# Kernel tuning notes

Measured on AMD Instinct MI355X. Metric: run time of the kernel, lower is better.

Reference implementation:

```python
import jax, jax.numpy as jnp
import numpy as np

N = 100000  # nodes
EPS_BN = 1e-5
EPS_NORM = 1e-12


def sage_conv(x, edge_index, wl, bl, wr):
    # PyG SAGEConv (aggr='mean', normalize=True, project=False):
    # out = lin_l(mean_{j in N(i)} x_j) + lin_r(x_i); then L2-normalize rows.
    src, dst = edge_index[0], edge_index[1]
    msgs = x[src]                                            # [E, C] gather
    agg = jax.ops.segment_sum(msgs, dst, num_segments=N)     # [N, C]
    cnt = jax.ops.segment_sum(jnp.ones((edge_index.shape[1],), x.dtype), dst,
                              num_segments=N)                # [N]
    agg = agg / jnp.maximum(cnt, 1.0)[:, None]               # mean (0 for isolated)
    out = agg @ wl.T + bl + x @ wr.T                         # lin_l has bias, lin_r doesn't
    nrm = jnp.sqrt(jnp.sum(out * out, axis=-1, keepdims=True))
    return out / jnp.maximum(nrm, EPS_NORM)


def batch_norm(x, gamma, beta):
    # BatchNorm1d in training mode: batch stats, biased variance
    mean = jnp.mean(x, axis=0)
    var = jnp.mean((x - mean) ** 2, axis=0)
    return gamma * (x - mean) * jax.lax.rsqrt(var + EPS_BN) + beta


def setup_inputs() -> dict:
    key = jax.random.key(0)
    ks = jax.random.split(key, 9)
    C_in, C_h, C_out = 128, 128, 47
    E = 800000
    x = jax.random.normal(ks[0], (N, C_in), dtype=jnp.float32)
    edge_index = jax.random.randint(ks[1], (2, E), 0, N, dtype=jnp.int64)
    s = 0.1
    return {
        "x": x,
        "edge_index": edge_index,
        "w1l": jax.random.normal(ks[2], (C_h, C_in), dtype=jnp.float32) * s,
        "b1l": jnp.zeros((C_h,), dtype=jnp.float32),
        "w1r": jax.random.normal(ks[3], (C_h, C_in), dtype=jnp.float32) * s,
        "bn_gamma": jnp.ones((C_h,), dtype=jnp.float32),
        "bn_beta": jnp.zeros((C_h,), dtype=jnp.float32),
        "w2l": jax.random.normal(ks[4], (C_out, C_h), dtype=jnp.float32) * s,
        "b2l": jnp.zeros((C_out,), dtype=jnp.float32),
        "w2r": jax.random.normal(ks[5], (C_out, C_h), dtype=jnp.float32) * s,
    }


def reference(x, edge_index, w1l, b1l, w1r, bn_gamma, bn_beta, w2l, b2l, w2r):
    h = sage_conv(x, edge_index, w1l, b1l, w1r)   # [N, 128]
    h = batch_norm(h, bn_gamma, bn_beta)
    h = jax.nn.relu(h)
    # dropout p=0.0 -> identity
    out = sage_conv(h, edge_index, w2l, b2l, w2r)  # [N, 47]
    return out
```

## Files before the change

### kernel.cpp

```cpp
#include <hip/hip_runtime.h>
#include <cstdint>


typedef __attribute__((ext_vector_type(8))) short s8v;
typedef __attribute__((ext_vector_type(4))) float fx4;

#define CSR_CHUNK 8192
#define CSR_SH 8
#define CSR_NBPAD 512
#define CSR_BUFCAP 3072

static __device__ __forceinline__ float bf2f(unsigned short h) {
    union { unsigned int u; float f; } c; c.u = (unsigned int)h << 16; return c.f;
}
static __device__ __forceinline__ unsigned short f2bf(float f) {
    union { float f; unsigned int u; } c; c.f = f;
    unsigned int u = c.u;
    return (unsigned short)((u + 0x7FFF + ((u >> 16) & 1)) >> 16);
}

static __device__ __forceinline__ float warp_sum64(float v) {
    #pragma unroll
    for (int off = 32; off > 0; off >>= 1) v += __shfl_xor(v, off, 64);
    return v;
}

__global__ __launch_bounds__(256) void k_prep(
        const float* __restrict__ x, const float* __restrict__ w1l,
        const float* __restrict__ w1r, const float* __restrict__ w2l,
        const float* __restrict__ w2r, const int* __restrict__ ei,
        unsigned short* __restrict__ xb, unsigned short* __restrict__ wB1,
        unsigned short* __restrict__ wB2p, float* __restrict__ stats,
        int* __restrict__ counts, int n, int nE, int prepBlocks) {
    __shared__ int hist[CSR_NBPAD];
    int t = threadIdx.x;
    if ((int)blockIdx.x >= prepBlocks) {
        int chunk = blockIdx.x - prepBlocks;
        hist[t] = 0; hist[t + 256] = 0;
        __syncthreads();
        int e0 = chunk * CSR_CHUNK;
        int e1 = min(e0 + CSR_CHUNK, nE);
        for (int e = e0 + t; e < e1; e += 256)
            atomicAdd(&hist[ei[nE + e] >> CSR_SH], 1);
        __syncthreads();
        counts[chunk * CSR_NBPAD + t] = hist[t];
        counts[chunk * CSR_NBPAD + t + 256] = hist[t + 256];
        return;
    }
    int idx = blockIdx.x * 256 + t;
    int nx = n * 16;
    if (idx < nx) {
        float4 a = ((const float4*)x)[idx * 2];
        float4 b = ((const float4*)x)[idx * 2 + 1];
        union { s8v v; unsigned short u[8]; } o;
        o.u[0] = f2bf(a.x); o.u[1] = f2bf(a.y); o.u[2] = f2bf(a.z); o.u[3] = f2bf(a.w);
        o.u[4] = f2bf(b.x); o.u[5] = f2bf(b.y); o.u[6] = f2bf(b.z); o.u[7] = f2bf(b.w);
        ((s8v*)xb)[idx] = o.v;
        return;
    }
    idx -= nx;
    if (idx < 32768) {
        int j = idx >> 8, k = idx & 255;
        float v = (k < 128) ? w1l[j * 128 + k] : w1r[j * 128 + (k - 128)];
        wB1[idx] = f2bf(v);
        return;
    }
    idx -= 32768;
    if (idx < 16384) {
        int j = idx >> 7, k = idx & 127;
        float v = 0.f;
        if (j < 47)      v = w2l[j * 128 + k];
        else if (j < 94) v = w2r[(j - 47) * 128 + k];
        wB2p[idx] = f2bf(v);
        return;
    }
    idx -= 16384;
    if (idx < 256) stats[idx] = 0.f;
}

__global__ __launch_bounds__(256) void k_bmeta(
        const int* __restrict__ counts, int* __restrict__ bucketStart,
        int* __restrict__ gcur, int nCh, int NB) {
    __shared__ int tot[CSR_NBPAD], tot2[CSR_NBPAD], sh[256], bs[CSR_NBPAD];
    int t = threadIdx.x;
    int tl = t & 127, g = t >> 7;
    int half = (nCh + 1) >> 1;
    int c0 = g * half, c1 = min(nCh, c0 + half);
    int4 s4 = {0, 0, 0, 0};
    for (int c = c0; c < c1; ++c) {
        int4 v = *(const int4*)(counts + (size_t)c * CSR_NBPAD + tl * 4);
        s4.x += v.x; s4.y += v.y; s4.z += v.z; s4.w += v.w;
    }
    *(int4*)((g ? tot2 : tot) + tl * 4) = s4;
    __syncthreads();
    tot[t] += tot2[t];
    tot[t + 256] += tot2[t + 256];
    __syncthreads();
    int pairSum = tot[2 * t] + tot[2 * t + 1];
    sh[t] = pairSum;
    __syncthreads();
    for (int off = 1; off < 256; off <<= 1) {
        int add = (t >= off) ? sh[t - off] : 0;
        __syncthreads();
        sh[t] += add;
        __syncthreads();
    }
    int excl = sh[t] - pairSum;
    bs[2 * t] = excl;
    bs[2 * t + 1] = excl + tot[2 * t];
    __syncthreads();
    for (int b = t; b <= NB; b += 256) bucketStart[b] = bs[b];
    for (int b = t; b < CSR_NBPAD; b += 256) gcur[b] = bs[b];
}

__global__ __launch_bounds__(256) void k_bfill(
        const int* __restrict__ ei, const int* __restrict__ counts,
        int* __restrict__ gcur, int* __restrict__ pairs, int nE) {
    __shared__ int cur[CSR_NBPAD];
    int t = threadIdx.x;
    #pragma unroll
    for (int i = 0; i < 2; ++i) {
        int b = t + i * 256;
        int h = counts[blockIdx.x * CSR_NBPAD + b];
        cur[b] = h ? atomicAdd(&gcur[b], h) : 0;
    }
    __syncthreads();
    int e0 = blockIdx.x * CSR_CHUNK;
    int e1 = min(e0 + CSR_CHUNK, nE);
    for (int e = e0 + t; e < e1; e += 256) {
        int s = ei[e];
        int d = ei[nE + e];
        int p = atomicAdd(&cur[d >> CSR_SH], 1);
        pairs[p] = (s << 8) | (d & 255);
    }
}

__global__ __launch_bounds__(256) void k_csr(
        const int* __restrict__ pairs, const int* __restrict__ bucketStart,
        int* __restrict__ deg, int* __restrict__ rowStart,
        int* __restrict__ srcIdx, int n) {
    __shared__ int cnt[256], scn[256], cur[256];
    __shared__ int buf[CSR_BUFCAP];
    int t = threadIdx.x;
    int bkt = blockIdx.x;
    int eBeg = bucketStart[bkt], eEnd = bucketStart[bkt + 1];
    int node0 = bkt << CSR_SH;
    cnt[t] = 0;
    __syncthreads();
    for (int e = eBeg + t; e < eEnd; e += 256)
        atomicAdd(&cnt[pairs[e] & 255], 1);
    __syncthreads();
    int myc = cnt[t];
    scn[t] = myc;
    __syncthreads();
    for (int off = 1; off < 256; off <<= 1) {
        int add = (t >= off) ? scn[t - off] : 0;
        __syncthreads();
        scn[t] += add;
        __syncthreads();
    }
    int excl = scn[t] - myc;
    cur[t] = excl;
    int node = node0 + t;
    if (node < n) { deg[node] = myc; rowStart[node] = eBeg + excl; }
    __syncthreads();
    for (int e = eBeg + t; e < eEnd; e += 256) {
        int pk = pairs[e];
        int p = atomicAdd(&cur[pk & 255], 1);
        int src = pk >> 8;
        if (p < CSR_BUFCAP) buf[p] = src;
        else srcIdx[eBeg + p] = src;
    }
    __syncthreads();
    int m = min(eEnd - eBeg, CSR_BUFCAP);
    for (int i = t; i < m; i += 256) srcIdx[eBeg + i] = buf[i];
}

__global__ __launch_bounds__(256) void k_gather1(
        const unsigned short* __restrict__ xb, const int* __restrict__ rowStart,
        const int* __restrict__ deg, const int* __restrict__ srcIdx,
        unsigned short* __restrict__ aggb, int n) {
    int t = threadIdx.x;
    int q = t & 15, grp = t >> 4;
    int node = blockIdx.x * 16 + grp;
    if (node >= n) return;
    int beg = rowStart[node];
    int d = deg[node];
    int end = beg + d;
    float a0[8] = {}, a1[8] = {}, a2[8] = {}, a3[8] = {};
    int e = beg;
    for (; e + 4 <= end; e += 4) {
        int s0 = srcIdx[e], s1v = srcIdx[e + 1], s2 = srcIdx[e + 2], s3 = srcIdx[e + 3];
        s8v v0 = *(const s8v*)(xb + (size_t)s0 * 128 + q * 8);
        s8v v1 = *(const s8v*)(xb + (size_t)s1v * 128 + q * 8);
        s8v v2 = *(const s8v*)(xb + (size_t)s2 * 128 + q * 8);
        s8v v3 = *(const s8v*)(xb + (size_t)s3 * 128 + q * 8);
        #pragma unroll
        for (int u = 0; u < 8; ++u) {
            a0[u] += bf2f((unsigned short)v0[u]);
            a1[u] += bf2f((unsigned short)v1[u]);
            a2[u] += bf2f((unsigned short)v2[u]);
            a3[u] += bf2f((unsigned short)v3[u]);
        }
    }
    for (; e < end; ++e) {
        s8v v0 = *(const s8v*)(xb + (size_t)srcIdx[e] * 128 + q * 8);
        #pragma unroll
        for (int u = 0; u < 8; ++u) a0[u] += bf2f((unsigned short)v0[u]);
    }
    float ic = 1.0f / fmaxf((float)d, 1.0f);
    union { s8v v; unsigned short u[8]; } o;
    #pragma unroll
    for (int u = 0; u < 8; ++u)
        o.u[u] = f2bf((a0[u] + a1[u] + a2[u] + a3[u]) * ic);
    *(s8v*)(aggb + (size_t)node * 128 + q * 8) = o.v;
}

__global__ __launch_bounds__(256, 3) void k_gemm1(
        const unsigned short* __restrict__ xb, const unsigned short* __restrict__ aggb,
        const unsigned short* __restrict__ wB1, const float* __restrict__ b1l,
        unsigned short* __restrict__ s1b, float* __restrict__ stats, int n) {
    __shared__ __align__(16) unsigned short xs[128 * 40];
    __shared__ __align__(16) unsigned short ws[128 * 40];
    int t = threadIdx.x;
    int w = t >> 6, L = t & 63;
    int q = L >> 4, lm = L & 15;
    int wr0 = (w >> 1) * 64;
    int wc0 = (w & 1) * 64;
    int r0 = blockIdx.x * 128;

    fx4 acc[4][4];
    fx4 z4 = {0.f, 0.f, 0.f, 0.f};
    #pragma unroll
    for (int r = 0; r < 4; ++r)
        #pragma unroll
        for (int c = 0; c < 4; ++c) acc[r][c] = z4;

    for (int kt = 0; kt < 8; ++kt) {
        const unsigned short* src = (kt < 4) ? aggb : xb;
        int kbase = (kt & 3) * 32;
        __syncthreads();
        #pragma unroll
        for (int it = 0; it < 2; ++it) {
            int i = t + it * 256;
            int row = i >> 2, kq = i & 3;
            int gr = r0 + row;
            s8v v = {0, 0, 0, 0, 0, 0, 0, 0};
            if (gr < n) v = *(const s8v*)(src + (size_t)gr * 128 + kbase + kq * 8);
            *(s8v*)&xs[row * 40 + kq * 8] = v;
            s8v wv = *(const s8v*)(wB1 + (size_t)row * 256 + kt * 32 + kq * 8);
            *(s8v*)&ws[row * 40 + kq * 8] = wv;
        }
        __syncthreads();
        s8v af[4], bf[4];
        #pragma unroll
        for (int r = 0; r < 4; ++r)
            af[r] = *(const s8v*)&xs[(wr0 + r * 16 + lm) * 40 + q * 8];
        #pragma unroll
        for (int c = 0; c < 4; ++c)
            bf[c] = *(const s8v*)&ws[(wc0 + c * 16 + lm) * 40 + q * 8];
        #pragma unroll
        for (int r = 0; r < 4; ++r)
            #pragma unroll
            for (int c = 0; c < 4; ++c)
                acc[r][c] = __builtin_amdgcn_mfma_f32_16x16x32_bf16(af[r], bf[c], acc[r][c], 0, 0, 0);
    }

    float bj[4];
    #pragma unroll
    for (int c = 0; c < 4; ++c) bj[c] = b1l[wc0 + c * 16 + lm];
    #pragma unroll
    for (int r = 0; r < 4; ++r)
        #pragma unroll
        for (int c = 0; c < 4; ++c) acc[r][c] += bj[c];

    fx4 pr[4];
    #pragma unroll
    for (int r = 0; r < 4; ++r) {
        fx4 p = acc[r][0] * acc[r][0];
        #pragma unroll
        for (int c = 1; c < 4; ++c) p += acc[r][c] * acc[r][c];
        #pragma unroll
        for (int off = 1; off <= 8; off <<= 1)
            #pragma unroll
            for (int i2 = 0; i2 < 4; ++i2) p[i2] += __shfl_xor(p[i2], off, 64);
        pr[r] = p;
    }

    __syncthreads();
    float* norm2 = (float*)xs;
    float* invn  = (float*)xs + 256;
    float* statS = (float*)ws;
    float* statQ = (float*)ws + 256;
    if (lm == 0) {
        #pragma unroll
        for (int r = 0; r < 4; ++r)
            #pragma unroll
            for (int i = 0; i < 4; ++i)
                norm2[(wr0 + r * 16 + q * 4 + i) * 2 + (w & 1)] = pr[r][i];
    }
    __syncthreads();
    if (t < 128) {
        float s = norm2[t * 2] + norm2[t * 2 + 1];
        invn[t] = 1.0f / fmaxf(sqrtf(s), 1e-12f);
    }
    __syncthreads();

    float cS[4] = {}, cQ[4] = {};
    #pragma unroll
    for (int r = 0; r < 4; ++r) {
        int rowb = wr0 + r * 16 + q * 4;
        fx4 iv = *(const fx4*)&invn[rowb];
        #pragma unroll
        for (int c = 0; c < 4; ++c) {
            fx4 v = acc[r][c] * iv;
            int col = wc0 + c * 16 + lm;
            #pragma unroll
            for (int i = 0; i < 4; ++i) {
                int gr = r0 + rowb + i;
                if (gr < n) {
                    s1b[(size_t)gr * 128 + col] = f2bf(v[i]);
                    cS[c] += v[i];
                    cQ[c] += v[i] * v[i];
                }
            }
        }
    }
    #pragma unroll
    for (int off = 16; off <= 32; off <<= 1)
        #pragma unroll
        for (int c = 0; c < 4; ++c) {
            cS[c] += __shfl_xor(cS[c], off, 64);
            cQ[c] += __shfl_xor(cQ[c], off, 64);
        }
    if (q == 0) {
        #pragma unroll
        for (int c = 0; c < 4; ++c) {
            int col = wc0 + c * 16 + lm;
            statS[col * 2 + (w >> 1)] = cS[c];
            statQ[col * 2 + (w >> 1)] = cQ[c];
        }
    }
    __syncthreads();
    if (t < 128) {
        atomicAdd(&stats[t],       statS[t * 2] + statS[t * 2 + 1]);
        atomicAdd(&stats[128 + t], statQ[t * 2] + statQ[t * 2 + 1]);
    }
}

__global__ __launch_bounds__(256, 3) void k_gemm2(
        const unsigned short* __restrict__ s1b, const unsigned short* __restrict__ wB2p,
        const float* __restrict__ stats, const float* __restrict__ gamma,
        const float* __restrict__ beta, const float* __restrict__ b2l,
        unsigned short* __restrict__ y2b, float* __restrict__ rbuf, int n) {
    __shared__ __align__(16) unsigned short xs[128 * 40];
    __shared__ __align__(16) unsigned short ws[128 * 40];
    __shared__ __align__(16) float abuf[128];
    __shared__ __align__(16) float bbuf[128];
    int t = threadIdx.x;
    int w = t >> 6, L = t & 63;
    int q = L >> 4, lm = L & 15;
    int wr0 = (w >> 1) * 64, wc0 = (w & 1) * 64;
    int r0 = blockIdx.x * 128;

    if (t < 128) {
        float s = stats[t], qv = stats[128 + t];
        float fn = (float)n;
        float mean = s / fn;
        float var = qv / fn - mean * mean;
        float istd = rsqrtf(var + 1e-5f);
        float a = gamma[t] * istd;
        abuf[t] = a;
        bbuf[t] = beta[t] - mean * a;
    }
    __syncthreads();

    fx4 acc[4][4];
    fx4 z4 = {0.f, 0.f, 0.f, 0.f};
    #pragma unroll
    for (int r = 0; r < 4; ++r)
        #pragma unroll
        for (int c = 0; c < 4; ++c) acc[r][c] = z4;

    for (int kt = 0; kt < 4; ++kt) {
        int kbase = kt * 32;
        __syncthreads();
        #pragma unroll
        for (int it = 0; it < 2; ++it) {
            int i = t + it * 256;
            int row = i >> 2, kq = i & 3;
            int gr = r0 + row;
            int cb = kbase + kq * 8;
            s8v v = {0, 0, 0, 0, 0, 0, 0, 0};
            if (gr < n) {
                s8v sv = *(const s8v*)(s1b + (size_t)gr * 128 + cb);
                fx4 a0 = *(const fx4*)&abuf[cb];
                fx4 a1 = *(const fx4*)&abuf[cb + 4];
                fx4 b0 = *(const fx4*)&bbuf[cb];
                fx4 b1 = *(const fx4*)&bbuf[cb + 4];
                union { s8v v; unsigned short u[8]; } o;
                #pragma unroll
                for (int u = 0; u < 4; ++u) {
                    float h0 = fmaxf(fmaf(a0[u], bf2f((unsigned short)sv[u]), b0[u]), 0.f);
                    float h1 = fmaxf(fmaf(a1[u], bf2f((unsigned short)sv[u + 4]), b1[u]), 0.f);
                    o.u[u]     = f2bf(h0);
                    o.u[u + 4] = f2bf(h1);
                }
                v = o.v;
            }
            *(s8v*)&xs[row * 40 + kq * 8] = v;
            s8v wv = *(const s8v*)(wB2p + (size_t)row * 128 + cb);
            *(s8v*)&ws[row * 40 + kq * 8] = wv;
        }
        __syncthreads();
        s8v af[4], bf[4];
        #pragma unroll
        for (int r = 0; r < 4; ++r)
            af[r] = *(const s8v*)&xs[(wr0 + r * 16 + lm) * 40 + q * 8];
        #pragma unroll
        for (int c = 0; c < 4; ++c)
            bf[c] = *(const s8v*)&ws[(wc0 + c * 16 + lm) * 40 + q * 8];
        #pragma unroll
        for (int r = 0; r < 4; ++r)
            #pragma unroll
            for (int c = 0; c < 4; ++c)
                acc[r][c] = __builtin_amdgcn_mfma_f32_16x16x32_bf16(af[r], bf[c], acc[r][c], 0, 0, 0);
    }

    #pragma unroll
    for (int c = 0; c < 4; ++c) {
        int col = wc0 + c * 16 + lm;
        float bb = (col >= 47 && col < 94) ? b2l[col - 47] : 0.f;
        #pragma unroll
        for (int r = 0; r < 4; ++r) {
            int rowb = wr0 + r * 16 + q * 4;
            #pragma unroll
            for (int i = 0; i < 4; ++i) {
                int gr = r0 + rowb + i;
                if (gr >= n) continue;
                float v = acc[r][c][i];
                if (col < 47)      y2b[(size_t)gr * 48 + col] = f2bf(v);
                else if (col < 94) rbuf[(size_t)gr * 47 + (col - 47)] = v + bb;
            }
        }
    }
}

__global__ __launch_bounds__(256) void k_gather2_final(
        const unsigned short* __restrict__ y2b, const float* __restrict__ rbuf,
        const int* __restrict__ rowStart, const int* __restrict__ deg,
        const int* __restrict__ srcIdx, float* __restrict__ out, int n) {
    int t = threadIdx.x;
    int lane = t & 63, w = t >> 6;
    int node = blockIdx.x * 4 + w;
    if (node >= n) return;
    int beg = rowStart[node];
    int d = deg[node];
    float v = 0.f;
    if (lane < 47) {
        int end = beg + d;
        float acc0 = 0.f, acc1 = 0.f, acc2 = 0.f, acc3 = 0.f;
        int e = beg;
        for (; e + 8 <= end; e += 8) {
            int s0 = srcIdx[e],     s1v = srcIdx[e + 1];
            int s2 = srcIdx[e + 2], s3  = srcIdx[e + 3];
            int s4 = srcIdx[e + 4], s5  = srcIdx[e + 5];
            int s6 = srcIdx[e + 6], s7  = srcIdx[e + 7];
            unsigned short l0 = y2b[(size_t)s0 * 48 + lane];
            unsigned short l1 = y2b[(size_t)s1v * 48 + lane];
            unsigned short l2 = y2b[(size_t)s2 * 48 + lane];
            unsigned short l3 = y2b[(size_t)s3 * 48 + lane];
            unsigned short l4 = y2b[(size_t)s4 * 48 + lane];
            unsigned short l5 = y2b[(size_t)s5 * 48 + lane];
            unsigned short l6 = y2b[(size_t)s6 * 48 + lane];
            unsigned short l7 = y2b[(size_t)s7 * 48 + lane];
            acc0 += bf2f(l0) + bf2f(l4);
            acc1 += bf2f(l1) + bf2f(l5);
            acc2 += bf2f(l2) + bf2f(l6);
            acc3 += bf2f(l3) + bf2f(l7);
        }
        for (; e + 4 <= end; e += 4) {
            int s0 = srcIdx[e], s1v = srcIdx[e + 1];
            int s2 = srcIdx[e + 2], s3 = srcIdx[e + 3];
            acc0 += bf2f(y2b[(size_t)s0 * 48 + lane]);
            acc1 += bf2f(y2b[(size_t)s1v * 48 + lane]);
            acc2 += bf2f(y2b[(size_t)s2 * 48 + lane]);
            acc3 += bf2f(y2b[(size_t)s3 * 48 + lane]);
        }
        for (; e < end; ++e) acc0 += bf2f(y2b[(size_t)srcIdx[e] * 48 + lane]);
        v = (acc0 + acc1 + acc2 + acc3) / fmaxf((float)d, 1.0f)
            + rbuf[(size_t)node * 47 + lane];
    }
    float ss = warp_sum64(v * v);
    float inv = 1.0f / fmaxf(sqrtf(ss), 1e-12f);
    if (lane < 47) out[(size_t)node * 47 + lane] = v * inv;
}

extern "C" void kernel_launch(void* const* d_in, const int* in_sizes, int n_in,
                              void* d_out, int out_size, void* d_ws, size_t ws_size,
                              hipStream_t stream) {
    const float* x     = (const float*)d_in[0];
    const int*   ei    = (const int*)d_in[1];
    const float* w1l   = (const float*)d_in[2];
    const float* b1l   = (const float*)d_in[3];
    const float* w1r   = (const float*)d_in[4];
    const float* gamma = (const float*)d_in[5];
    const float* beta  = (const float*)d_in[6];
    const float* w2l   = (const float*)d_in[7];
    const float* b2l   = (const float*)d_in[8];
    const float* w2r   = (const float*)d_in[9];
    float* out = (float*)d_out;

    int n  = in_sizes[0] / 128;
    int nE = in_sizes[1] / 2;

    int NB  = (n + 255) >> 8;
    int nCh = (nE + CSR_CHUNK - 1) / CSR_CHUNK;

    int* deg       = (int*)d_ws;
    float* stats   = (float*)(deg + n);
    int* rowStart  = (int*)(stats + 256);
    int* meta      = rowStart + n;
    int* srcIdx    = meta + n;
    unsigned short* xb   = (unsigned short*)(srcIdx + nE);
    unsigned short* aggb = xb + (size_t)n * 128;
    unsigned short* s1b  = aggb + (size_t)n * 128;
    unsigned short* wB1  = s1b + (size_t)n * 128;
    unsigned short* wB2p = wB1 + 32768;
    int* counts      = meta;
    int* bucketStart = meta + 60000;
    int* gcur        = meta + 61000;
    int* pairs       = (int*)s1b;
    unsigned short* y2b = xb;
    float* rbuf = (float*)(y2b + (size_t)n * 48);

    int prepTotal  = n * 16 + 32768 + 16384 + 256;
    int prepBlocks = (prepTotal + 255) / 256;

    k_prep<<<prepBlocks + nCh, 256, 0, stream>>>(
        x, w1l, w1r, w2l, w2r, ei, xb, wB1, wB2p, stats, counts, n, nE, prepBlocks);
    k_bmeta<<<1, 256, 0, stream>>>(counts, bucketStart, gcur, nCh, NB);
    k_bfill<<<nCh, 256, 0, stream>>>(ei, counts, gcur, pairs, nE);
    k_csr<<<NB, 256, 0, stream>>>(pairs, bucketStart, deg, rowStart, srcIdx, n);
    k_gather1<<<(n + 15) / 16, 256, 0, stream>>>(xb, rowStart, deg, srcIdx, aggb, n);
    k_gemm1<<<(n + 127) / 128, 256, 0, stream>>>(xb, aggb, wB1, b1l, s1b, stats, n);
    k_gemm2<<<(n + 127) / 128, 256, 0, stream>>>(
        s1b, wB2p, stats, gamma, beta, b2l, y2b, rbuf, n);
    k_gather2_final<<<(n + 3) / 4, 256, 0, stream>>>(y2b, rbuf, rowStart, deg, srcIdx, out, n);
}
```

Measured before the change: 299.2 us.

## Load GEMM tiles directly into swizzled LDS via global_load_lds

```diff
diff --git a/kernel.cpp b/kernel.cpp
--- a/kernel.cpp
+++ b/kernel.cpp
@@ -216,12 +216,17 @@
     *(s8v*)(aggb + (size_t)node * 128 + q * 8) = o.v;
 }
 
+#define GLL16(GSRC, LDST) \
+    __builtin_amdgcn_global_load_lds( \
+        (__attribute__((address_space(1))) void*)(void*)(GSRC), \
+        (__attribute__((address_space(3))) void*)(LDST), 16, 0, 0)
+
 __global__ __launch_bounds__(256, 3) void k_gemm1(
         const unsigned short* __restrict__ xb, const unsigned short* __restrict__ aggb,
         const unsigned short* __restrict__ wB1, const float* __restrict__ b1l,
         unsigned short* __restrict__ s1b, float* __restrict__ stats, int n) {
-    __shared__ __align__(16) unsigned short xs[128 * 40];
-    __shared__ __align__(16) unsigned short ws[128 * 40];
+    __shared__ __align__(16) unsigned short xs[128 * 32];
+    __shared__ __align__(16) unsigned short ws[128 * 32];
     int t = threadIdx.x;
     int w = t >> 6, L = t & 63;
     int q = L >> 4, lm = L & 15;
@@ -243,27 +248,29 @@
         #pragma unroll
         for (int it = 0; it < 2; ++it) {
             int i = t + it * 256;
-            int row = i >> 2, kq = i & 3;
-            int gr = r0 + row;
-            s8v v = {0, 0, 0, 0, 0, 0, 0, 0};
-            if (gr < n) v = *(const s8v*)(src + (size_t)gr * 128 + kbase + kq * 8);
-            *(s8v*)&xs[row * 40 + kq * 8] = v;
-            s8v wv = *(const s8v*)(wB1 + (size_t)row * 256 + kt * 32 + kq * 8);
-            *(s8v*)&ws[row * 40 + kq * 8] = wv;
-        }
-        __syncthreads();
-        s8v af[4], bf[4];
+            int row = i >> 2, p = i & 3;
+            int sl = p ^ ((row >> 1) & 3);
+            int gr = r0 + row; gr = gr < n ? gr : (n - 1);
+            GLL16(src + (size_t)gr * 128 + kbase + sl * 8, &xs[i * 8]);
+            GLL16(wB1 + (size_t)row * 256 + kt * 32 + sl * 8, &ws[i * 8]);
+        }
+        __syncthreads();
+        s8v af[4], bfr[4];
+        #pragma unroll
+        for (int r = 0; r < 4; ++r) {
+            int row = wr0 + r * 16 + lm;
+            af[r] = *(const s8v*)&xs[row * 32 + ((q ^ ((row >> 1) & 3)) << 3)];
+        }
+        #pragma unroll
+        for (int c = 0; c < 4; ++c) {
+            int row = wc0 + c * 16 + lm;
+            bfr[c] = *(const s8v*)&ws[row * 32 + ((q ^ ((row >> 1) & 3)) << 3)];
+        }
         #pragma unroll
         for (int r = 0; r < 4; ++r)
-            af[r] = *(const s8v*)&xs[(wr0 + r * 16 + lm) * 40 + q * 8];
-        #pragma unroll
-        for (int c = 0; c < 4; ++c)
-            bf[c] = *(const s8v*)&ws[(wc0 + c * 16 + lm) * 40 + q * 8];
-        #pragma unroll
-        for (int r = 0; r < 4; ++r)
             #pragma unroll
             for (int c = 0; c < 4; ++c)
-                acc[r][c] = __builtin_amdgcn_mfma_f32_16x16x32_bf16(af[r], bf[c], acc[r][c], 0, 0, 0);
+                acc[r][c] = __builtin_amdgcn_mfma_f32_16x16x32_bf16(af[r], bfr[c], acc[r][c], 0, 0, 0);
     }
 
     float bj[4];
@@ -353,8 +360,8 @@
         const float* __restrict__ stats, const float* __restrict__ gamma,
         const float* __restrict__ beta, const float* __restrict__ b2l,
         unsigned short* __restrict__ y2b, float* __restrict__ rbuf, int n) {
-    __shared__ __align__(16) unsigned short xs[128 * 40];
-    __shared__ __align__(16) unsigned short ws[128 * 40];
+    __shared__ __align__(16) unsigned short xs[128 * 32];
+    __shared__ __align__(16) unsigned short ws[128 * 32];
     __shared__ __align__(16) float abuf[128];
     __shared__ __align__(16) float bbuf[128];
     int t = threadIdx.x;
@@ -388,43 +395,42 @@
         #pragma unroll
         for (int it = 0; it < 2; ++it) {
             int i = t + it * 256;
-            int row = i >> 2, kq = i & 3;
-            int gr = r0 + row;
-            int cb = kbase + kq * 8;
-            s8v v = {0, 0, 0, 0, 0, 0, 0, 0};
-            if (gr < n) {
-                s8v sv = *(const s8v*)(s1b + (size_t)gr * 128 + cb);
-                fx4 a0 = *(const fx4*)&abuf[cb];
-                fx4 a1 = *(const fx4*)&abuf[cb + 4];
-                fx4 b0 = *(const fx4*)&bbuf[cb];
-                fx4 b1 = *(const fx4*)&bbuf[cb + 4];
-                union { s8v v; unsigned short u[8]; } o;
-                #pragma unroll
-                for (int u = 0; u < 4; ++u) {
-                    float h0 = fmaxf(fmaf(a0[u], bf2f((unsigned short)sv[u]), b0[u]), 0.f);
-                    float h1 = fmaxf(fmaf(a1[u], bf2f((unsigned short)sv[u + 4]), b1[u]), 0.f);
-                    o.u[u]     = f2bf(h0);
-                    o.u[u + 4] = f2bf(h1);
-                }
-                v = o.v;
+            int row = i >> 2, p = i & 3;
+            int sl = p ^ ((row >> 1) & 3);
+            int gr = r0 + row; gr = gr < n ? gr : (n - 1);
+            GLL16(s1b + (size_t)gr * 128 + kbase + sl * 8, &xs[i * 8]);
+            GLL16(wB2p + (size_t)row * 128 + kbase + sl * 8, &ws[i * 8]);
+        }
+        __syncthreads();
+        fx4 a0 = *(const fx4*)&abuf[kbase + q * 8];
+        fx4 a1 = *(const fx4*)&abuf[kbase + q * 8 + 4];
+        fx4 b0 = *(const fx4*)&bbuf[kbase + q * 8];
+        fx4 b1 = *(const fx4*)&bbuf[kbase + q * 8 + 4];
+        s8v af[4], bfr[4];
+        #pragma unroll
+        for (int r = 0; r < 4; ++r) {
+            int row = wr0 + r * 16 + lm;
+            s8v sv = *(const s8v*)&xs[row * 32 + ((q ^ ((row >> 1) & 3)) << 3)];
+            union { s8v v; unsigned short u[8]; } o;
+            #pragma unroll
+            for (int u = 0; u < 4; ++u) {
+                float h0 = fmaxf(fmaf(a0[u], bf2f((unsigned short)sv[u]), b0[u]), 0.f);
+                float h1 = fmaxf(fmaf(a1[u], bf2f((unsigned short)sv[u + 4]), b1[u]), 0.f);
+                o.u[u]     = f2bf(h0);
+                o.u[u + 4] = f2bf(h1);
             }
-            *(s8v*)&xs[row * 40 + kq * 8] = v;
-            s8v wv = *(const s8v*)(wB2p + (size_t)row * 128 + cb);
-            *(s8v*)&ws[row * 40 + kq * 8] = wv;
-        }
-        __syncthreads();
-        s8v af[4], bf[4];
+            af[r] = o.v;
+        }
+        #pragma unroll
+        for (int c = 0; c < 4; ++c) {
+            int row = wc0 + c * 16 + lm;
+            bfr[c] = *(const s8v*)&ws[row * 32 + ((q ^ ((row >> 1) & 3)) << 3)];
+        }
         #pragma unroll
         for (int r = 0; r < 4; ++r)
-            af[r] = *(const s8v*)&xs[(wr0 + r * 16 + lm) * 40 + q * 8];
-        #pragma unroll
-        for (int c = 0; c < 4; ++c)
-            bf[c] = *(const s8v*)&ws[(wc0 + c * 16 + lm) * 40 + q * 8];
-        #pragma unroll
-        for (int r = 0; r < 4; ++r)
             #pragma unroll
             for (int c = 0; c < 4; ++c)
-                acc[r][c] = __builtin_amdgcn_mfma_f32_16x16x32_bf16(af[r], bf[c], acc[r][c], 0, 0, 0);
+                acc[r][c] = __builtin_amdgcn_mfma_f32_16x16x32_bf16(af[r], bfr[c], acc[r][c], 0, 0, 0);
     }
 
     #pragma unroll
```

Result: faster. 288.7 us (-3.5%).
